# Performance work log

Measured on AMD Instinct MI355X. Metric: run time of the kernel, lower is better.

## Reference

```python
import jax, jax.numpy as jnp
import numpy as np

BLOCK = 64  # quantization block size along in_features
IN, OUT, RANK, ALPHA = 4096, 4096, 16, 32
SCALING = ALPHA / RANK


def setup_inputs() -> dict:
    key = jax.random.key(0)
    ks = jax.random.split(key, 6)
    x = jax.random.normal(ks[0], (8, 1024, IN), dtype=jnp.float32)
    # int4 codes in [0, 15]; dequant subtracts 8 -> [-8, 7]
    qweight = jax.random.randint(ks[1], (OUT, IN), 0, 16, dtype=jnp.int32)
    # blockwise absmax-style scales, small positive
    scales = jax.random.uniform(ks[2], (OUT, IN // BLOCK), dtype=jnp.float32) * 0.02 + 1e-3
    bias = jax.random.normal(ks[3], (OUT,), dtype=jnp.float32) * 0.02
    lora_A = jax.random.normal(ks[4], (IN, RANK), dtype=jnp.float32) * 0.02
    lora_B = jnp.zeros((RANK, OUT), dtype=jnp.float32)
    return {"x": x, "qweight": qweight, "scales": scales, "bias": bias,
            "lora_A": lora_A, "lora_B": lora_B}


def _dequant(qweight, scales):
    # qweight: [out, in] int codes in [0,15]; scales: [out, in/BLOCK]
    out, in_f = qweight.shape
    q = (qweight.astype(jnp.float32) - 8.0).reshape(out, in_f // BLOCK, BLOCK)
    return (q * scales[:, :, None]).reshape(out, in_f)  # [out, in]


def reference(x, qweight, scales, bias, lora_A, lora_B):
    W = _dequant(qweight, scales)                      # [out, in]
    base = jnp.einsum('bsi,oi->bso', x, W) + bias      # quantized linear
    lora = jnp.einsum('bsr,ro->bso', jnp.einsum('bsi,ir->bsr', x, lora_A), lora_B)
    return base + lora * SCALING
```

## Files before the change

kernel.cpp:

```cpp
#include <hip/hip_runtime.h>
#include <hip/hip_bf16.h>

#define IN_F 4096
#define OUT_F 4096
#define M_TOK 8192
#define RANK 16

typedef __attribute__((ext_vector_type(4))) float f32x4;
typedef __attribute__((ext_vector_type(8))) short short8;

struct alignas(16) bf16x8_s { __hip_bfloat16 v[8]; };

#define CONV_BLOCKS 2048
#define CONV_ITERS (M_TOK * IN_F / (8 * 256 * CONV_BLOCKS))

__global__ __launch_bounds__(256) void conv_kernel(
    const float* __restrict__ x,
    __hip_bfloat16* __restrict__ xb) {
    size_t idx = (size_t)blockIdx.x * 256 + threadIdx.x;
    const size_t stride = (size_t)CONV_BLOCKS * 256;
#pragma unroll
    for (int it = 0; it < CONV_ITERS; ++it, idx += stride) {
        const size_t base = idx * 8;
        float4 v0 = *(const float4*)(x + base);
        float4 v1 = *(const float4*)(x + base + 4);
        bf16x8_s r;
        r.v[0] = __float2bfloat16(v0.x);
        r.v[1] = __float2bfloat16(v0.y);
        r.v[2] = __float2bfloat16(v0.z);
        r.v[3] = __float2bfloat16(v0.w);
        r.v[4] = __float2bfloat16(v1.x);
        r.v[5] = __float2bfloat16(v1.y);
        r.v[6] = __float2bfloat16(v1.z);
        r.v[7] = __float2bfloat16(v1.w);
        *(bf16x8_s*)(xb + base) = r;
    }
}

#define DEQ_BLOCKS 2048

__global__ __launch_bounds__(256) void deq_kernel(
    const int* __restrict__ q,
    const float* __restrict__ scales,
    const float* __restrict__ lA,
    const float* __restrict__ lB,
    __hip_bfloat16* __restrict__ W) {
    const int tid = threadIdx.x;
    const int bid = blockIdx.x;
    const int o0 = (bid >> 1) * 4;
    const int i0 = (bid & 1) * 2048 + tid * 8;

    float bw[16][4];
#pragma unroll
    for (int r = 0; r < 16; ++r)
#pragma unroll
        for (int oi = 0; oi < 4; ++oi)
            bw[r][oi] = 2.0f * lB[(size_t)r * OUT_F + o0 + oi];

    float fold[4][8];
#pragma unroll
    for (int e = 0; e < 8; ++e) {
        const float* ar = lA + (size_t)(i0 + e) * RANK;
        float4 a0 = *(const float4*)(ar + 0);
        float4 a1 = *(const float4*)(ar + 4);
        float4 a2 = *(const float4*)(ar + 8);
        float4 a3 = *(const float4*)(ar + 12);
#pragma unroll
        for (int oi = 0; oi < 4; ++oi) {
            float f = a0.x * bw[0][oi] + a0.y * bw[1][oi]
                    + a0.z * bw[2][oi] + a0.w * bw[3][oi]
                    + a1.x * bw[4][oi] + a1.y * bw[5][oi]
                    + a1.z * bw[6][oi] + a1.w * bw[7][oi]
                    + a2.x * bw[8][oi] + a2.y * bw[9][oi]
                    + a2.z * bw[10][oi] + a2.w * bw[11][oi]
                    + a3.x * bw[12][oi] + a3.y * bw[13][oi]
                    + a3.z * bw[14][oi] + a3.w * bw[15][oi];
            fold[oi][e] = f;
        }
    }

#pragma unroll
    for (int oi = 0; oi < 4; ++oi) {
        const int o = o0 + oi;
        const float s = scales[o * 64 + (i0 >> 6)];
        const int4* qp = (const int4*)(q + (size_t)o * IN_F + i0);
        int4 q0 = qp[0];
        int4 q1 = qp[1];
        bf16x8_s r;
        r.v[0] = __float2bfloat16(s * (float)(q0.x - 8) + fold[oi][0]);
        r.v[1] = __float2bfloat16(s * (float)(q0.y - 8) + fold[oi][1]);
        r.v[2] = __float2bfloat16(s * (float)(q0.z - 8) + fold[oi][2]);
        r.v[3] = __float2bfloat16(s * (float)(q0.w - 8) + fold[oi][3]);
        r.v[4] = __float2bfloat16(s * (float)(q1.x - 8) + fold[oi][4]);
        r.v[5] = __float2bfloat16(s * (float)(q1.y - 8) + fold[oi][5]);
        r.v[6] = __float2bfloat16(s * (float)(q1.z - 8) + fold[oi][6]);
        r.v[7] = __float2bfloat16(s * (float)(q1.w - 8) + fold[oi][7]);
        *(bf16x8_s*)(W + (size_t)o * IN_F + i0) = r;
    }
}

#define BK 64
#define NT (IN_F / BK)

__device__ __forceinline__ short8 ldfrag(const short* p, int half, int row, int gran) {
    return *(const short8*)(p + half * 8192 + row * 64 + ((gran ^ (row & 7)) * 8));
}

#define STAGE(LDSbuf, SRC, ROW0, K0)                                          \
    {                                                                         \
        _Pragma("unroll")                                                     \
        for (int j = 0; j < 2; ++j) {                                         \
            const __hip_bfloat16* g = (SRC) +                                 \
                (size_t)((ROW0) + j * 64 + wave * 8 + srow) * IN_F + (K0) + sgc; \
            __builtin_amdgcn_global_load_lds(                                 \
                (const __attribute__((address_space(1))) void*)g,             \
                (__attribute__((address_space(3))) void*)((LDSbuf) + (j * 64 + wave * 8) * 64), \
                16, 0, 0);                                                    \
        }                                                                     \
    }

#define RD_A(BUF, HALF, KG)                                                   \
    _Pragma("unroll") for (int f = 0; f < 4; ++f)                             \
        fa[f] = ldfrag(BUF, HALF, wm * 64 + f * 16 + fr, (KG) * 4 + fc);

#define RD_B(BUF, KG)                                                         \
    _Pragma("unroll") for (int g2 = 0; g2 < 4; ++g2)                          \
        fb[g2] = ldfrag(BUF, bhalf, brow0 + g2 * 16 + fr, (KG) * 4 + fc);

#define MFMA16(MH)                                                            \
    _Pragma("unroll") for (int f = 0; f < 4; ++f)                             \
    _Pragma("unroll") for (int g2 = 0; g2 < 4; ++g2)                          \
        acc[(MH) * 4 + f][g2] = __builtin_amdgcn_mfma_f32_16x16x32_bf16(      \
            fa[f], fb[g2], acc[(MH) * 4 + f][g2], 0, 0, 0);

#define BAR __builtin_amdgcn_s_barrier();

__global__ __launch_bounds__(512, 2) void qlora_gemm_kernel(
    const __hip_bfloat16* __restrict__ xb,
    const __hip_bfloat16* __restrict__ Wq,
    const float* __restrict__ bias,
    float* __restrict__ out) {
    __shared__ __hip_bfloat16 As[2][16384];
    __shared__ __hip_bfloat16 Bs[2][16384];

    const int tid  = threadIdx.x;
    const int wave = tid >> 6;
    const int lane = tid & 63;
    const int wm = wave >> 2;
    const int wn = wave & 3;

    const int wg = ((int)blockIdx.x & 7) * 32 + ((int)blockIdx.x >> 3);
    const int bx = wg & 15;
    const int by = wg >> 4;
    const int m0 = by * 256;
    const int n0 = bx * 256;

    f32x4 acc[8][4];
#pragma unroll
    for (int i = 0; i < 8; ++i)
#pragma unroll
        for (int j = 0; j < 4; ++j)
            acc[i][j] = (f32x4){0.f, 0.f, 0.f, 0.f};

    const int srow = lane >> 3;
    const int sgc  = ((lane & 7) ^ srow) * 8;

    const int fr = lane & 15;
    const int fc = lane >> 4;

    const int bhalf = wn >> 1;
    const int brow0 = (wn & 1) * 64;

    const short* A0p = (const short*)As[0];
    const short* A1p = (const short*)As[1];
    const short* B0p = (const short*)Bs[0];
    const short* B1p = (const short*)Bs[1];

    short8 fa[4];
    short8 fb[4];

    STAGE(As[0],        xb, m0,       0);
    STAGE(As[0] + 8192, xb, m0 + 128, 0);
    STAGE(Bs[0],        Wq, n0,       0);
    STAGE(Bs[0] + 8192, Wq, n0 + 128, 0);
    STAGE(As[1],        xb, m0,       BK);
    STAGE(Bs[1],        Wq, n0,       BK);
    asm volatile("s_waitcnt vmcnt(4)" ::: "memory");

    for (int it = 0; it < NT / 2; ++it) {
        const int t = it * 2;
        const int k_t1 = (t + 1) * BK;
        const int k_t2 = ((t + 2) & (NT - 1)) * BK;
        const int k_t3 = ((t + 3) & (NT - 1)) * BK;

        BAR RD_A(A0p, 0, 0) RD_B(B0p, 0)
            STAGE(As[1] + 8192, xb, m0 + 128, k_t1)
            MFMA16(0)
        BAR RD_A(A0p, 1, 0)
            STAGE(Bs[1] + 8192, Wq, n0 + 128, k_t1)
            MFMA16(1)
        BAR RD_A(A0p, 0, 1) RD_B(B0p, 1)
            MFMA16(0)
        BAR RD_A(A0p, 1, 1)
            STAGE(As[0], xb, m0, k_t2)
            STAGE(Bs[0], Wq, n0, k_t2)
            MFMA16(1)
        asm volatile("s_waitcnt vmcnt(4)" ::: "memory");

        BAR RD_A(A1p, 0, 0) RD_B(B1p, 0)
            STAGE(As[0] + 8192, xb, m0 + 128, k_t2)
            MFMA16(0)
        BAR RD_A(A1p, 1, 0)
            STAGE(Bs[0] + 8192, Wq, n0 + 128, k_t2)
            MFMA16(1)
        BAR RD_A(A1p, 0, 1) RD_B(B1p, 1)
            MFMA16(0)
        BAR RD_A(A1p, 1, 1)
            STAGE(As[1], xb, m0, k_t3)
            STAGE(Bs[1], Wq, n0, k_t3)
            MFMA16(1)
        asm volatile("s_waitcnt vmcnt(4)" ::: "memory");
    }

    asm volatile("s_waitcnt vmcnt(0)" ::: "memory");

    const int cc  = lane & 15;
    const int rr4 = (lane >> 4) * 4;
    float bv[4];
#pragma unroll
    for (int g2 = 0; g2 < 4; ++g2)
        bv[g2] = bias[n0 + wn * 64 + g2 * 16 + cc];

#pragma unroll
    for (int mh = 0; mh < 2; ++mh)
#pragma unroll
        for (int f = 0; f < 4; ++f) {
            const int m = m0 + mh * 128 + wm * 64 + f * 16 + rr4;
#pragma unroll
            for (int g2 = 0; g2 < 4; ++g2) {
                const int n = n0 + wn * 64 + g2 * 16 + cc;
                float* op = out + (size_t)m * OUT_F + n;
                const f32x4 a = acc[mh * 4 + f][g2];
#pragma unroll
                for (int r = 0; r < 4; ++r)
                    op[(size_t)r * OUT_F] = a[r] + bv[g2];
            }
        }
}

extern "C" void kernel_launch(void* const* d_in, const int* in_sizes, int n_in,
                              void* d_out, int out_size, void* d_ws, size_t ws_size,
                              hipStream_t stream) {
    const float* x      = (const float*)d_in[0];
    const int*   qw     = (const int*)  d_in[1];
    const float* scales = (const float*)d_in[2];
    const float* bias   = (const float*)d_in[3];
    const float* lA     = (const float*)d_in[4];
    const float* lB     = (const float*)d_in[5];
    float* out = (float*)d_out;

    char* ws = (char*)d_ws;
    __hip_bfloat16* Wq = (__hip_bfloat16*)ws;
    __hip_bfloat16* xb = (__hip_bfloat16*)(ws + (size_t)32 * 1024 * 1024);

    conv_kernel<<<CONV_BLOCKS, 256, 0, stream>>>(x, xb);
    deq_kernel<<<DEQ_BLOCKS, 256, 0, stream>>>(qw, scales, lA, lB, Wq);
    const size_t half = (size_t)4096 * IN_F;
    const size_t ohalf = (size_t)4096 * OUT_F;
    qlora_gemm_kernel<<<dim3(256), dim3(512), 0, stream>>>(xb, Wq, bias, out);
    qlora_gemm_kernel<<<dim3(256), dim3(512), 0, stream>>>(xb + half, Wq, bias, out + ohalf);
}
```

Baseline: 582.0 us.

## Fuse fp32-to-bf16 activation conversion into GEMM A-tile staging

Removes the separate conversion kernel. The GEMM now loads fp32 activations into registers, converts them to bf16 and writes them into swizzled LDS, instead of DMA-loading a pre-converted bf16 copy. This drops a full pass over x (read fp32, write bf16, re-read bf16) and one launch. In exchange the GEMM reads twice as many bytes for A on every tile, uses more VGPRs for the staging registers, and adds VALU/LDS-write work that may interfere with the MFMA pipeline and its waitcnt scheme.

```diff
diff --git a/kernel.cpp b/kernel.cpp
--- a/kernel.cpp
+++ b/kernel.cpp
@@ -10,32 +10,6 @@
 typedef __attribute__((ext_vector_type(8))) short short8;
 
 struct alignas(16) bf16x8_s { __hip_bfloat16 v[8]; };
-
-#define CONV_BLOCKS 2048
-#define CONV_ITERS (M_TOK * IN_F / (8 * 256 * CONV_BLOCKS))
-
-__global__ __launch_bounds__(256) void conv_kernel(
-    const float* __restrict__ x,
-    __hip_bfloat16* __restrict__ xb) {
-    size_t idx = (size_t)blockIdx.x * 256 + threadIdx.x;
-    const size_t stride = (size_t)CONV_BLOCKS * 256;
-#pragma unroll
-    for (int it = 0; it < CONV_ITERS; ++it, idx += stride) {
-        const size_t base = idx * 8;
-        float4 v0 = *(const float4*)(x + base);
-        float4 v1 = *(const float4*)(x + base + 4);
-        bf16x8_s r;
-        r.v[0] = __float2bfloat16(v0.x);
-        r.v[1] = __float2bfloat16(v0.y);
-        r.v[2] = __float2bfloat16(v0.z);
-        r.v[3] = __float2bfloat16(v0.w);
-        r.v[4] = __float2bfloat16(v1.x);
-        r.v[5] = __float2bfloat16(v1.y);
-        r.v[6] = __float2bfloat16(v1.z);
-        r.v[7] = __float2bfloat16(v1.w);
-        *(bf16x8_s*)(xb + base) = r;
-    }
-}
 
 #define DEQ_BLOCKS 2048
 
@@ -106,11 +80,11 @@
     return *(const short8*)(p + half * 8192 + row * 64 + ((gran ^ (row & 7)) * 8));
 }
 
-#define STAGE(LDSbuf, SRC, ROW0, K0)                                          \
+#define STAGE_B(LDSbuf, ROW0, K0)                                             \
     {                                                                         \
         _Pragma("unroll")                                                     \
         for (int j = 0; j < 2; ++j) {                                         \
-            const __hip_bfloat16* g = (SRC) +                                 \
+            const __hip_bfloat16* g = Wq +                                    \
                 (size_t)((ROW0) + j * 64 + wave * 8 + srow) * IN_F + (K0) + sgc; \
             __builtin_amdgcn_global_load_lds(                                 \
                 (const __attribute__((address_space(1))) void*)g,             \
@@ -119,6 +93,37 @@
         }                                                                     \
     }
 
+#define LOAD_A_F32(K0)                                                        \
+    {                                                                         \
+        _Pragma("unroll")                                                     \
+        for (int h = 0; h < 2; ++h)                                           \
+        _Pragma("unroll")                                                     \
+        for (int j = 0; j < 2; ++j) {                                         \
+            const float* gp = xf +                                            \
+                (size_t)(m0 + h * 128 + j * 64 + wave * 8 + srow) * IN_F +    \
+                (K0) + (lane & 7) * 8;                                        \
+            axf[h * 2 + j][0] = *(const float4*)gp;                           \
+            axf[h * 2 + j][1] = *(const float4*)(gp + 4);                     \
+        }                                                                     \
+    }
+
+#define WRITE_A(DSTBUF, H)                                                    \
+    {                                                                         \
+        _Pragma("unroll")                                                     \
+        for (int j = 0; j < 2; ++j) {                                         \
+            bf16x8_s pk;                                                      \
+            const float4 u0 = axf[(H) * 2 + j][0];                            \
+            const float4 u1 = axf[(H) * 2 + j][1];                            \
+            pk.v[0] = __float2bfloat16(u0.x); pk.v[1] = __float2bfloat16(u0.y); \
+            pk.v[2] = __float2bfloat16(u0.z); pk.v[3] = __float2bfloat16(u0.w); \
+            pk.v[4] = __float2bfloat16(u1.x); pk.v[5] = __float2bfloat16(u1.y); \
+            pk.v[6] = __float2bfloat16(u1.z); pk.v[7] = __float2bfloat16(u1.w); \
+            __hip_bfloat16* dst = (DSTBUF) + (H) * 8192 +                     \
+                (j * 64 + wave * 8 + srow) * 64 + ((lane & 7) ^ srow) * 8;    \
+            *(bf16x8_s*)dst = pk;                                             \
+        }                                                                     \
+    }
+
 #define RD_A(BUF, HALF, KG)                                                   \
     _Pragma("unroll") for (int f = 0; f < 4; ++f)                             \
         fa[f] = ldfrag(BUF, HALF, wm * 64 + f * 16 + fr, (KG) * 4 + fc);
@@ -136,7 +141,7 @@
 #define BAR __builtin_amdgcn_s_barrier();
 
 __global__ __launch_bounds__(512, 2) void qlora_gemm_kernel(
-    const __hip_bfloat16* __restrict__ xb,
+    const float* __restrict__ xf,
     const __hip_bfloat16* __restrict__ Wq,
     const float* __restrict__ bias,
     float* __restrict__ out) {
@@ -178,14 +183,16 @@
 
     short8 fa[4];
     short8 fb[4];
-
-    STAGE(As[0],        xb, m0,       0);
-    STAGE(As[0] + 8192, xb, m0 + 128, 0);
-    STAGE(Bs[0],        Wq, n0,       0);
-    STAGE(Bs[0] + 8192, Wq, n0 + 128, 0);
-    STAGE(As[1],        xb, m0,       BK);
-    STAGE(Bs[1],        Wq, n0,       BK);
-    asm volatile("s_waitcnt vmcnt(4)" ::: "memory");
+    float4 axf[4][2];
+
+    LOAD_A_F32(0);
+    STAGE_B(Bs[0],        n0,       0);
+    STAGE_B(Bs[0] + 8192, n0 + 128, 0);
+    STAGE_B(Bs[1],        n0,       BK);
+    WRITE_A(As[0], 0);
+    WRITE_A(As[0], 1);
+    asm volatile("s_waitcnt lgkmcnt(0)" ::: "memory");
+    asm volatile("s_waitcnt vmcnt(2)" ::: "memory");
 
     for (int it = 0; it < NT / 2; ++it) {
         const int t = it * 2;
@@ -194,32 +201,36 @@
         const int k_t3 = ((t + 3) & (NT - 1)) * BK;
 
         BAR RD_A(A0p, 0, 0) RD_B(B0p, 0)
-            STAGE(As[1] + 8192, xb, m0 + 128, k_t1)
+            LOAD_A_F32(k_t1)
             MFMA16(0)
         BAR RD_A(A0p, 1, 0)
-            STAGE(Bs[1] + 8192, Wq, n0 + 128, k_t1)
+            STAGE_B(Bs[1] + 8192, n0 + 128, k_t1)
             MFMA16(1)
         BAR RD_A(A0p, 0, 1) RD_B(B0p, 1)
+            WRITE_A((__hip_bfloat16*)As[1], 0)
             MFMA16(0)
         BAR RD_A(A0p, 1, 1)
-            STAGE(As[0], xb, m0, k_t2)
-            STAGE(Bs[0], Wq, n0, k_t2)
-            MFMA16(1)
-        asm volatile("s_waitcnt vmcnt(4)" ::: "memory");
+            STAGE_B(Bs[0], n0, k_t2)
+            WRITE_A((__hip_bfloat16*)As[1], 1)
+            MFMA16(1)
+        asm volatile("s_waitcnt lgkmcnt(0)" ::: "memory");
+        asm volatile("s_waitcnt vmcnt(2)" ::: "memory");
 
         BAR RD_A(A1p, 0, 0) RD_B(B1p, 0)
-            STAGE(As[0] + 8192, xb, m0 + 128, k_t2)
+            LOAD_A_F32(k_t2)
             MFMA16(0)
         BAR RD_A(A1p, 1, 0)
-            STAGE(Bs[0] + 8192, Wq, n0 + 128, k_t2)
+            STAGE_B(Bs[0] + 8192, n0 + 128, k_t2)
             MFMA16(1)
         BAR RD_A(A1p, 0, 1) RD_B(B1p, 1)
+            WRITE_A((__hip_bfloat16*)As[0], 0)
             MFMA16(0)
         BAR RD_A(A1p, 1, 1)
-            STAGE(As[1], xb, m0, k_t3)
-            STAGE(Bs[1], Wq, n0, k_t3)
-            MFMA16(1)
-        asm volatile("s_waitcnt vmcnt(4)" ::: "memory");
+            STAGE_B(Bs[1], n0, k_t3)
+            WRITE_A((__hip_bfloat16*)As[0], 1)
+            MFMA16(1)
+        asm volatile("s_waitcnt lgkmcnt(0)" ::: "memory");
+        asm volatile("s_waitcnt vmcnt(2)" ::: "memory");
     }
 
     asm volatile("s_waitcnt vmcnt(0)" ::: "memory");
@@ -259,14 +270,11 @@
     const float* lB     = (const float*)d_in[5];
     float* out = (float*)d_out;
 
-    char* ws = (char*)d_ws;
-    __hip_bfloat16* Wq = (__hip_bfloat16*)ws;
-    __hip_bfloat16* xb = (__hip_bfloat16*)(ws + (size_t)32 * 1024 * 1024);
-
-    conv_kernel<<<CONV_BLOCKS, 256, 0, stream>>>(x, xb);
+    __hip_bfloat16* Wq = (__hip_bfloat16*)d_ws;
+
     deq_kernel<<<DEQ_BLOCKS, 256, 0, stream>>>(qw, scales, lA, lB, Wq);
-    const size_t half = (size_t)4096 * IN_F;
+    const size_t xhalf = (size_t)4096 * IN_F;
     const size_t ohalf = (size_t)4096 * OUT_F;
-    qlora_gemm_kernel<<<dim3(256), dim3(512), 0, stream>>>(xb, Wq, bias, out);
-    qlora_gemm_kernel<<<dim3(256), dim3(512), 0, stream>>>(xb + half, Wq, bias, out + ohalf);
-}
+    qlora_gemm_kernel<<<dim3(256), dim3(512), 0, stream>>>(x, Wq, bias, out);
+    qlora_gemm_kernel<<<dim3(256), dim3(512), 0, stream>>>(x + xhalf, Wq, bias, out + ohalf);
+}
```

New measurement: 663.4 us. 14.0% more time.
